# Kernel optimization log

Measured on AMD Instinct MI355X. Metric: run time of the kernel, lower is better.

## Reference

```python
import jax, jax.numpy as jnp
import numpy as np

N, E, D_IN, D_H, D_OUT = 100000, 1600000, 128, 128, 16


def setup_inputs() -> dict:
    key = jax.random.key(0)
    k_x, k_e, k_w1, k_w2 = jax.random.split(key, 4)
    x = jax.random.normal(k_x, (N, D_IN), dtype=jnp.float32)
    edge_index = jax.random.randint(k_e, (2, E), 0, N, dtype=jnp.int64)
    # glorot-ish init for the two GCNConv weight matrices
    W1 = jax.random.normal(k_w1, (D_IN, D_H), dtype=jnp.float32) * (1.0 / np.sqrt(D_IN))
    b1 = jnp.zeros((D_H,), dtype=jnp.float32)
    W2 = jax.random.normal(k_w2, (D_H, D_OUT), dtype=jnp.float32) * (1.0 / np.sqrt(D_H))
    b2 = jnp.zeros((D_OUT,), dtype=jnp.float32)
    return {"x": x, "edge_index": edge_index, "W1": W1, "b1": b1, "W2": W2, "b2": b2}


def _gcn_conv(x, src, dst, norm, W, b, n):
    # linear transform, gather from source nodes, normalize, scatter-add to targets
    h = x @ W                                   # [N, d_out]
    msg = h[src] * norm[:, None]                # [E+N, d_out]
    return jax.ops.segment_sum(msg, dst, num_segments=n) + b


def reference(x, edge_index, W1, b1, W2, b2):
    n = x.shape[0]
    # GCNConv default: add self-loops, symmetric normalization D^-1/2 A D^-1/2
    loops = jnp.arange(n, dtype=edge_index.dtype)
    src = jnp.concatenate([edge_index[0], loops])
    dst = jnp.concatenate([edge_index[1], loops])
    deg = jax.ops.segment_sum(jnp.ones_like(dst, dtype=x.dtype), dst, num_segments=n)
    dinv = jnp.where(deg > 0, jax.lax.rsqrt(deg), 0.0)
    norm = dinv[src] * dinv[dst]                # [E+N]

    h = _gcn_conv(x, src, dst, norm, W1, b1, n)
    h = jax.nn.relu(h)
    # dropout is identity in eval mode (reference uses eval / deterministic path)
    out = _gcn_conv(h, src, dst, norm, W2, b2, n)
    return out
```

## Files before the change

### kernel.cpp

```cpp
#include <hip/hip_runtime.h>

typedef unsigned int uint;
typedef __attribute__((ext_vector_type(8))) short bf16x8;
typedef __attribute__((ext_vector_type(4))) float f32x4;

#define D_IN 128
#define D_H  128
#define D_OUT 16
#define NPC 512
#define NPCSH 9
#define CLDS 224
#define P1 256
#define XL_STRIDE 68
#define WT_STRIDE 68

static __device__ __forceinline__ float bflo(uint u) { return __uint_as_float(u << 16); }
static __device__ __forceinline__ float bfhi(uint u) { return __uint_as_float(u & 0xFFFF0000u); }
static __device__ __forceinline__ uint f2bf(float f) {
    uint b = __float_as_uint(f);
    return (b + 0x7FFFu + ((b >> 16) & 1u)) >> 16;
}
static __device__ __forceinline__ uint pk(float a, float b) {
    return f2bf(a) | (f2bf(b) << 16);
}


__global__ __launch_bounds__(256) void k_p1hist(const int* __restrict__ dst, int E, int N, int C,
                                                int chunk, int* __restrict__ hist1,
                                                const float* __restrict__ W1,
                                                uint* __restrict__ W1p) {
    __shared__ int h[CLDS];
    int t = threadIdx.x, b = blockIdx.x;
    if (b >= P1) {
        int p = (b - P1) * 256 + t;
        int k2 = p >> 7, f = p & 127;
        float w0 = W1[(size_t)(2 * k2) * 128 + f];
        float w1 = W1[(size_t)(2 * k2 + 1) * 128 + f];
        W1p[p] = pk(w0, w1);
        return;
    }
    for (int i = t; i < C; i += 256) h[i] = 0;
    __syncthreads();
    int e0 = b * chunk, e1 = min(e0 + chunk, E);
    for (int e = e0 + t; e < e1; e += 256) {
        int d = dst[e];
        d = max(0, min(d, N - 1));
        atomicAdd(&h[d >> NPCSH], 1);
    }
    __syncthreads();
    for (int i = t; i < C; i += 256) hist1[(size_t)i * P1 + b] = h[i];
}

__global__ __launch_bounds__(1024) void k_p1scan(int* __restrict__ hist1, int C,
                                                 int* __restrict__ cbase) {
    __shared__ int col[CLDS];
    __shared__ int sdata[1024];
    int t = threadIdx.x;
    int w = t >> 6, lane = t & 63;
    for (int i = w; i < C; i += 16) {
        int4 v = ((const int4*)hist1)[i * 64 + lane];
        int s = v.x + v.y + v.z + v.w;
        int inc = s;
        for (int off = 1; off < 64; off <<= 1) {
            int o = __shfl_up(inc, off);
            if (lane >= off) inc += o;
        }
        int excl = inc - s;
        int4 p;
        p.x = excl;
        p.y = excl + v.x;
        p.z = excl + v.x + v.y;
        p.w = excl + v.x + v.y + v.z;
        ((int4*)hist1)[i * 64 + lane] = p;
        if (lane == 63) col[i] = inc;
    }
    __syncthreads();
    int v = (t < C) ? col[t] : 0;
    sdata[t] = v;
    __syncthreads();
    for (int off = 1; off < 1024; off <<= 1) {
        int x = (t >= off) ? sdata[t - off] : 0;
        __syncthreads();
        sdata[t] += x;
        __syncthreads();
    }
    int pos = sdata[t] - v;
    if (t < C) cbase[t] = pos;
    if (t == 1023) cbase[C] = sdata[1023];
    if (t < C) col[t] = pos;
    __syncthreads();
    for (int i = w; i < C; i += 16) {
        int base = col[i];
        int4 p = ((int4*)hist1)[i * 64 + lane];
        p.x += base; p.y += base; p.z += base; p.w += base;
        ((int4*)hist1)[i * 64 + lane] = p;
    }
}

__global__ __launch_bounds__(256) void k_p1fill(const int* __restrict__ src,
                                                const int* __restrict__ dst, int E, int N, int C,
                                                int chunk, const int* __restrict__ hist1,
                                                uint* __restrict__ binned1) {
    __shared__ int cur[CLDS];
    int t = threadIdx.x, b = blockIdx.x;
    for (int i = t; i < C; i += 256) cur[i] = hist1[(size_t)i * P1 + b];
    __syncthreads();
    int e0 = b * chunk, e1 = min(e0 + chunk, E);
    for (int e = e0 + t; e < e1; e += 256) {
        int d = dst[e];
        d = max(0, min(d, N - 1));
        int s = src[e];
        s = max(0, min(s, N - 1));
        int p = atomicAdd(&cur[d >> NPCSH], 1);
        binned1[p] = ((uint)(d & (NPC - 1)) << 17) | (uint)s;
    }
}


__global__ __launch_bounds__(256) void k_p2gemm1(const uint* __restrict__ binned1,
                                                 const int* __restrict__ cbase, int N, int C,
                                                 int* __restrict__ ssrc, int* __restrict__ rowptr,
                                                 int* __restrict__ deg, float* __restrict__ dinv,
                                                 const uint* __restrict__ W1p,
                                                 const float* __restrict__ x,
                                                 uint* __restrict__ hs_b, int ntiles) {
    __shared__ uint smem[128 * WT_STRIDE + 64 * XL_STRIDE];
    int t = threadIdx.x;
    if ((int)blockIdx.x < C) {
        int* ncnt = (int*)smem;
        int* nbase_ = ncnt + NPC;
        int* sdata = nbase_ + NPC;
        int c = blockIdx.x;
        int start = cbase[c], end = cbase[c + 1];
        for (int i = t; i < NPC; i += 256) ncnt[i] = 0;
        __syncthreads();
        for (int j = start + t; j < end; j += 256) atomicAdd(&ncnt[binned1[j] >> 17], 1);
        __syncthreads();
        int v0 = ncnt[2 * t], v1 = ncnt[2 * t + 1];
        int s = v0 + v1;
        sdata[t] = s;
        __syncthreads();
        for (int off = 1; off < 256; off <<= 1) {
            int xv = (t >= off) ? sdata[t - off] : 0;
            __syncthreads();
            sdata[t] += xv;
            __syncthreads();
        }
        int pre = sdata[t] - s;
        nbase_[2 * t] = start + pre;
        nbase_[2 * t + 1] = start + pre + v0;
        __syncthreads();
        for (int i = t; i < NPC; i += 256) {
            int node = c * NPC + i;
            if (node < N) {
                deg[node] = ncnt[i];
                rowptr[node] = nbase_[i];
                dinv[node] = rsqrtf((float)ncnt[i] + 1.0f);
            }
        }
        __syncthreads();
        for (int i = t; i < NPC; i += 256) ncnt[i] = nbase_[i];
        __syncthreads();
        for (int j = start + t; j < end; j += 256) {
            uint pe = binned1[j];
            int p = atomicAdd(&ncnt[pe >> 17], 1);
            ssrc[p] = (int)(pe & 0x1FFFFu);
        }
        return;
    }
    uint* Wt = smem;
    uint* xl = smem + 128 * WT_STRIDE;
    int role = blockIdx.x - C;
    int nroles = gridDim.x - C;
    for (int p = t; p < 64 * 128; p += 256) {
        int k2 = p >> 7, f = p & 127;
        Wt[f * WT_STRIDE + k2] = W1p[p];
    }
    int w = t >> 6, lane = t & 63;
    int q = lane >> 4, m = lane & 15;
    const float4* x4 = (const float4*)x;
    for (int tile = role; tile < ntiles; tile += nroles) {
        int row0 = tile * 64;
        __syncthreads();
        for (int p = t; p < 64 * 32; p += 256) {
            int r = p >> 5, c2 = p & 31;
            int gr = row0 + r;
            float4 v = (gr < N) ? x4[(size_t)gr * 32 + c2] : make_float4(0.f, 0.f, 0.f, 0.f);
            *(uint2*)&xl[r * XL_STRIDE + 2 * c2] = make_uint2(pk(v.x, v.y), pk(v.z, v.w));
        }
        __syncthreads();
        bf16x8 afr[4][4];
#pragma unroll
        for (int rt = 0; rt < 4; rt++)
#pragma unroll
            for (int kc = 0; kc < 4; kc++)
                afr[rt][kc] = *(const bf16x8*)&xl[(rt * 16 + m) * XL_STRIDE + kc * 16 + q * 4];
        f32x4 acc[2][4];
#pragma unroll
        for (int c = 0; c < 2; c++)
#pragma unroll
            for (int rt = 0; rt < 4; rt++) acc[c][rt] = (f32x4){0.f, 0.f, 0.f, 0.f};
#pragma unroll
        for (int c = 0; c < 2; c++) {
            int f = w * 32 + c * 16 + m;
#pragma unroll
            for (int kc = 0; kc < 4; kc++) {
                bf16x8 bfr = *(const bf16x8*)&Wt[f * WT_STRIDE + kc * 16 + q * 4];
#pragma unroll
                for (int rt = 0; rt < 4; rt++)
                    acc[c][rt] = __builtin_amdgcn_mfma_f32_16x16x32_bf16(afr[rt][kc], bfr,
                                                                         acc[c][rt], 0, 0, 0);
            }
        }
        __syncthreads();
        uint* outl = xl;
#pragma unroll
        for (int rt = 0; rt < 4; rt++) {
#pragma unroll
            for (int c = 0; c < 2; c++) {
                f32x4 a = acc[c][rt];
#pragma unroll
                for (int r = 0; r < 4; r++) {
                    float v = a[r];
                    float vn = __shfl_xor(v, 1);
                    if (!(lane & 1)) {
                        int row = rt * 16 + q * 4 + r;
                        int cp = (w * 32 + c * 16 + m) >> 1;
                        outl[row * 65 + cp] = pk(v, vn);
                    }
                }
            }
        }
        __syncthreads();
        for (int p = t; p < 64 * 64; p += 256) {
            int r = p >> 6, cc = p & 63;
            int gr = row0 + r;
            if (gr < N) hs_b[(size_t)gr * 64 + cc] = outl[r * 65 + cc];
        }
    }
}


__global__ __launch_bounds__(256) void k_agg1(const uint* __restrict__ hs_b,
                                              const int* __restrict__ rowptr,
                                              const int* __restrict__ deg,
                                              const int* __restrict__ ssrc,
                                              const float* __restrict__ dinv,
                                              const float2* __restrict__ b1, int N,
                                              uint* __restrict__ rh_b) {
    int w = threadIdx.x >> 6, lane = threadIdx.x & 63;
    int d = blockIdx.x * 4 + w;
    if (d >= N) return;
    int start = rowptr[d], cnt = deg[d];
    float sc = dinv[d];
    uint sv = hs_b[(size_t)d * 64 + lane];
    float a0 = bflo(sv) * sc, a1 = bfhi(sv) * sc;
    int base = 0;
    while (base < cnt) {
        int nb = min(cnt - base, 64);
        int idxv = (lane < nb) ? ssrc[start + base + lane] : 0;
        float dvv = dinv[idxv];
        int j = 0;
        for (; j + 16 <= nb; j += 16) {
            uint u[16];
            float dv[16];
#pragma unroll
            for (int q = 0; q < 16; q++) {
                int i = __shfl(idxv, j + q);
                dv[q] = __shfl(dvv, j + q);
                u[q] = hs_b[(size_t)i * 64 + lane];
            }
#pragma unroll
            for (int q = 0; q < 16; q++) {
                a0 = fmaf(bflo(u[q]), dv[q], a0);
                a1 = fmaf(bfhi(u[q]), dv[q], a1);
            }
        }
        for (; j + 4 <= nb; j += 4) {
            uint u[4];
            float dv[4];
#pragma unroll
            for (int q = 0; q < 4; q++) {
                int i = __shfl(idxv, j + q);
                dv[q] = __shfl(dvv, j + q);
                u[q] = hs_b[(size_t)i * 64 + lane];
            }
#pragma unroll
            for (int q = 0; q < 4; q++) {
                a0 = fmaf(bflo(u[q]), dv[q], a0);
                a1 = fmaf(bfhi(u[q]), dv[q], a1);
            }
        }
        for (; j < nb; j++) {
            int i = __shfl(idxv, j);
            float dv = __shfl(dvv, j);
            uint u = hs_b[(size_t)i * 64 + lane];
            a0 = fmaf(bflo(u), dv, a0);
            a1 = fmaf(bfhi(u), dv, a1);
        }
        base += nb;
    }
    float2 bb = b1[lane];
    rh_b[(size_t)d * 64 + lane] =
        pk(fmaxf(fmaf(a0, sc, bb.x), 0.f), fmaxf(fmaf(a1, sc, bb.y), 0.f));
}


__global__ __launch_bounds__(256) void k_gemm2(const uint* __restrict__ rh_b,
                                               const float* __restrict__ W2,
                                               const float* __restrict__ dinv, int N,
                                               uint* __restrict__ h2_b) {
    __shared__ float Wl[D_H * D_OUT];
    int t = threadIdx.x;
    for (int i = t; i < D_H * D_OUT; i += 256) Wl[i] = W2[i];
    __syncthreads();
    int r = blockIdx.x * 256 + t;
    if (r >= N) return;
    const uint* xrow = rh_b + (size_t)r * 64;
    float acc[16];
#pragma unroll
    for (int f = 0; f < 16; f++) acc[f] = 0.f;
    for (int c = 0; c < 16; c++) {
        uint4 xv = *(const uint4*)(xrow + c * 4);
        uint xs[4] = {xv.x, xv.y, xv.z, xv.w};
#pragma unroll
        for (int u = 0; u < 4; u++) {
            int k = c * 8 + u * 2;
            float x0 = bflo(xs[u]), x1 = bfhi(xs[u]);
            const float* w0 = &Wl[k * 16];
            const float* w1 = &Wl[(k + 1) * 16];
#pragma unroll
            for (int f = 0; f < 16; f++) acc[f] = fmaf(x0, w0[f], acc[f]);
#pragma unroll
            for (int f = 0; f < 16; f++) acc[f] = fmaf(x1, w1[f], acc[f]);
        }
    }
    float sc = dinv[r];
    uint o[8];
#pragma unroll
    for (int q = 0; q < 8; q++) o[q] = pk(acc[2 * q] * sc, acc[2 * q + 1] * sc);
    *(uint4*)&h2_b[(size_t)r * 8] = make_uint4(o[0], o[1], o[2], o[3]);
    *(uint4*)&h2_b[(size_t)r * 8 + 4] = make_uint4(o[4], o[5], o[6], o[7]);
}


__global__ __launch_bounds__(256) void k_agg2(const uint* __restrict__ h2_b,
                                              const int* __restrict__ rowptr,
                                              const int* __restrict__ deg,
                                              const int* __restrict__ ssrc,
                                              const float* __restrict__ dinv,
                                              const float* __restrict__ b2, int N,
                                              float2* __restrict__ out) {
    int w = threadIdx.x >> 6, lane = threadIdx.x & 63;
    int d = blockIdx.x * 4 + w;
    if (d >= N) return;
    int slot = lane >> 3, jp = lane & 7;
    int start = rowptr[d], cnt = deg[d];
    float a0 = 0.f, a1 = 0.f;
    if (slot == 0) {
        uint sv = h2_b[(size_t)d * 8 + jp];
        a0 = bflo(sv);
        a1 = bfhi(sv);
    }
    int base = 0;
    while (base < cnt) {
        int nb = min(cnt - base, 64);
        int idxv = (lane < nb) ? ssrc[start + base + lane] : 0;
        int ng = (nb + 7) >> 3;
        if (ng <= 4) {
            int i0 = __shfl(idxv, slot);
            int i1 = __shfl(idxv, 8 + slot);
            int i2 = __shfl(idxv, 16 + slot);
            int i3 = __shfl(idxv, 24 + slot);
            uint u0 = (slot < nb) ? h2_b[(size_t)i0 * 8 + jp] : 0u;
            uint u1 = (8 + slot < nb) ? h2_b[(size_t)i1 * 8 + jp] : 0u;
            uint u2 = (16 + slot < nb) ? h2_b[(size_t)i2 * 8 + jp] : 0u;
            uint u3 = (24 + slot < nb) ? h2_b[(size_t)i3 * 8 + jp] : 0u;
            a0 += bflo(u0) + bflo(u1) + bflo(u2) + bflo(u3);
            a1 += bfhi(u0) + bfhi(u1) + bfhi(u2) + bfhi(u3);
        } else {
            for (int g = 0; g < ng; g++) {
                int j = g * 8 + slot;
                int i = __shfl(idxv, j);
                if (j < nb) {
                    uint hv = h2_b[(size_t)i * 8 + jp];
                    a0 += bflo(hv);
                    a1 += bfhi(hv);
                }
            }
        }
        base += nb;
    }
    a0 += __shfl_xor(a0, 8);
    a1 += __shfl_xor(a1, 8);
    a0 += __shfl_xor(a0, 16);
    a1 += __shfl_xor(a1, 16);
    a0 += __shfl_xor(a0, 32);
    a1 += __shfl_xor(a1, 32);
    if (slot == 0) {
        float di = dinv[d];
        out[(size_t)d * 8 + jp] =
            make_float2(fmaf(a0, di, b2[2 * jp]), fmaf(a1, di, b2[2 * jp + 1]));
    }
}


extern "C" void kernel_launch(void* const* d_in, const int* in_sizes, int n_in,
                              void* d_out, int out_size, void* d_ws, size_t ws_size,
                              hipStream_t stream) {
    const float* x  = (const float*)d_in[0];
    const int*   ei = (const int*)d_in[1];
    const float* W1 = (const float*)d_in[2];
    const float* b1 = (const float*)d_in[3];
    const float* W2 = (const float*)d_in[4];
    const float* b2 = (const float*)d_in[5];
    int N = in_sizes[0] / D_IN;
    int E = in_sizes[1] / 2;
    const int* src = ei;
    const int* dst = ei + E;
    int C = (N + NPC - 1) / NPC;
    int chunk = (E + P1 - 1) / P1;
    int ntiles = (N + 63) / 64;

    char* ws = (char*)d_ws;
    size_t off = 0;
    auto alloc = [&](size_t bytes) -> char* {
        char* p = ws + off;
        off = (off + bytes + 255) & ~(size_t)255;
        return p;
    };
    int*   hist1   = (int*)alloc((size_t)P1 * C * 4);
    int*   cbase   = (int*)alloc((size_t)(C + 1) * 4);
    uint*  binned1 = (uint*)alloc((size_t)E * 4);
    int*   ssrc    = (int*)alloc((size_t)E * 4);
    int*   rowptr  = (int*)alloc((size_t)N * 4);
    int*   deg     = (int*)alloc((size_t)N * 4);
    float* dinv    = (float*)alloc((size_t)N * 4);
    uint*  W1p     = (uint*)alloc((size_t)64 * 128 * 4);
    uint*  hs_b    = (uint*)alloc((size_t)N * 64 * 4);
    uint*  rh_b    = (uint*)alloc((size_t)N * 64 * 4);
    uint*  h2_b    = hs_b;

    k_p1hist<<<P1 + 32, 256, 0, stream>>>(dst, E, N, C, chunk, hist1, W1, W1p);
    k_p1scan<<<1, 1024, 0, stream>>>(hist1, C, cbase);
    k_p1fill<<<P1, 256, 0, stream>>>(src, dst, E, N, C, chunk, hist1, binned1);
    int g1 = min(768, ntiles);
    k_p2gemm1<<<C + g1, 256, 0, stream>>>(binned1, cbase, N, C, ssrc, rowptr, deg, dinv,
                                          W1p, x, hs_b, ntiles);
    k_agg1<<<(N + 3) / 4, 256, 0, stream>>>(hs_b, rowptr, deg, ssrc, dinv,
                                            (const float2*)b1, N, rh_b);
    k_gemm2<<<(N + 255) / 256, 256, 0, stream>>>(rh_b, W2, dinv, N, h2_b);
    k_agg2<<<(N + 3) / 4, 256, 0, stream>>>(h2_b, rowptr, deg, ssrc, dinv, b2, N,
                                            (float2*)d_out);
}
```

Before: 278.5 us.

## Pre-scale GEMM1 output by dinv and fuse layer-2 GEMM into aggregation

A separate degree kernel now computes deg and dinv before GEMM1, so GEMM1 can scale each output row by dinv[src]. Because rows arrive pre-scaled, the first aggregation drops the per-edge dinv gather and shuffle and becomes a plain sum. That aggregation also applies the 128x16 W2 projection in registers with a wave-wide shuffle reduction, removing the k_gemm2 kernel and the full write and read of the 128-wide relu output. The cost is an extra launch plus a second pass over binned1, and 16 shuffle reductions of six steps each per node.

New measurement: 332.5 us. 1.19x slower.

```diff
diff --git a/kernel.cpp b/kernel.cpp
--- a/kernel.cpp
+++ b/kernel.cpp
@@ -117,10 +117,30 @@
 }
 
 
+__global__ __launch_bounds__(256) void k_deg(const uint* __restrict__ binned1,
+                                             const int* __restrict__ cbase, int N,
+                                             int* __restrict__ deg, float* __restrict__ dinv) {
+    __shared__ int ncnt[NPC];
+    int c = blockIdx.x, t = threadIdx.x;
+    int start = cbase[c], end = cbase[c + 1];
+    for (int i = t; i < NPC; i += 256) ncnt[i] = 0;
+    __syncthreads();
+    for (int j = start + t; j < end; j += 256) atomicAdd(&ncnt[binned1[j] >> 17], 1);
+    __syncthreads();
+    for (int i = t; i < NPC; i += 256) {
+        int node = c * NPC + i;
+        if (node < N) {
+            deg[node] = ncnt[i];
+            dinv[node] = rsqrtf((float)ncnt[i] + 1.0f);
+        }
+    }
+}
+
+
 __global__ __launch_bounds__(256) void k_p2gemm1(const uint* __restrict__ binned1,
                                                  const int* __restrict__ cbase, int N, int C,
                                                  int* __restrict__ ssrc, int* __restrict__ rowptr,
-                                                 int* __restrict__ deg, float* __restrict__ dinv,
+                                                 const float* __restrict__ dinv,
                                                  const uint* __restrict__ W1p,
                                                  const float* __restrict__ x,
                                                  uint* __restrict__ hs_b, int ntiles) {
@@ -152,11 +172,7 @@
         __syncthreads();
         for (int i = t; i < NPC; i += 256) {
             int node = c * NPC + i;
-            if (node < N) {
-                deg[node] = ncnt[i];
-                rowptr[node] = nbase_[i];
-                dinv[node] = rsqrtf((float)ncnt[i] + 1.0f);
-            }
+            if (node < N) rowptr[node] = nbase_[i];
         }
         __syncthreads();
         for (int i = t; i < NPC; i += 256) ncnt[i] = nbase_[i];
@@ -216,12 +232,23 @@
         uint* outl = xl;
 #pragma unroll
         for (int rt = 0; rt < 4; rt++) {
+            int gb = row0 + rt * 16 + q * 4;
+            float4 dv;
+            if (gb + 3 < N) {
+                dv = *(const float4*)&dinv[gb];
+            } else {
+                dv.x = (gb < N) ? dinv[gb] : 0.f;
+                dv.y = (gb + 1 < N) ? dinv[gb + 1] : 0.f;
+                dv.z = (gb + 2 < N) ? dinv[gb + 2] : 0.f;
+                dv.w = (gb + 3 < N) ? dinv[gb + 3] : 0.f;
+            }
+            float dr[4] = {dv.x, dv.y, dv.z, dv.w};
 #pragma unroll
             for (int c = 0; c < 2; c++) {
                 f32x4 a = acc[c][rt];
 #pragma unroll
                 for (int r = 0; r < 4; r++) {
-                    float v = a[r];
+                    float v = a[r] * dr[r];
                     float vn = __shfl_xor(v, 1);
                     if (!(lane & 1)) {
                         int row = rt * 16 + q * 4 + r;
@@ -241,106 +268,80 @@
 }
 
 
-__global__ __launch_bounds__(256) void k_agg1(const uint* __restrict__ hs_b,
-                                              const int* __restrict__ rowptr,
-                                              const int* __restrict__ deg,
-                                              const int* __restrict__ ssrc,
-                                              const float* __restrict__ dinv,
-                                              const float2* __restrict__ b1, int N,
-                                              uint* __restrict__ rh_b) {
+__global__ __launch_bounds__(256) void k_agg1g2(const uint* __restrict__ hs_b,
+                                                const int* __restrict__ rowptr,
+                                                const int* __restrict__ deg,
+                                                const int* __restrict__ ssrc,
+                                                const float* __restrict__ dinv,
+                                                const float2* __restrict__ b1,
+                                                const float* __restrict__ W2, int N,
+                                                uint* __restrict__ h2_b) {
     int w = threadIdx.x >> 6, lane = threadIdx.x & 63;
     int d = blockIdx.x * 4 + w;
     if (d >= N) return;
     int start = rowptr[d], cnt = deg[d];
-    float sc = dinv[d];
     uint sv = hs_b[(size_t)d * 64 + lane];
-    float a0 = bflo(sv) * sc, a1 = bfhi(sv) * sc;
+    float a0 = bflo(sv), a1 = bfhi(sv);
     int base = 0;
     while (base < cnt) {
         int nb = min(cnt - base, 64);
         int idxv = (lane < nb) ? ssrc[start + base + lane] : 0;
-        float dvv = dinv[idxv];
         int j = 0;
         for (; j + 16 <= nb; j += 16) {
             uint u[16];
-            float dv[16];
 #pragma unroll
             for (int q = 0; q < 16; q++) {
                 int i = __shfl(idxv, j + q);
-                dv[q] = __shfl(dvv, j + q);
                 u[q] = hs_b[(size_t)i * 64 + lane];
             }
 #pragma unroll
             for (int q = 0; q < 16; q++) {
-                a0 = fmaf(bflo(u[q]), dv[q], a0);
-                a1 = fmaf(bfhi(u[q]), dv[q], a1);
+                a0 += bflo(u[q]);
+                a1 += bfhi(u[q]);
             }
         }
         for (; j + 4 <= nb; j += 4) {
             uint u[4];
-            float dv[4];
 #pragma unroll
             for (int q = 0; q < 4; q++) {
                 int i = __shfl(idxv, j + q);
-                dv[q] = __shfl(dvv, j + q);
                 u[q] = hs_b[(size_t)i * 64 + lane];
             }
 #pragma unroll
             for (int q = 0; q < 4; q++) {
-                a0 = fmaf(bflo(u[q]), dv[q], a0);
-                a1 = fmaf(bfhi(u[q]), dv[q], a1);
+                a0 += bflo(u[q]);
+                a1 += bfhi(u[q]);
             }
         }
         for (; j < nb; j++) {
             int i = __shfl(idxv, j);
-            float dv = __shfl(dvv, j);
             uint u = hs_b[(size_t)i * 64 + lane];
-            a0 = fmaf(bflo(u), dv, a0);
-            a1 = fmaf(bfhi(u), dv, a1);
+            a0 += bflo(u);
+            a1 += bfhi(u);
         }
         base += nb;
     }
+    float sc = dinv[d];
     float2 bb = b1[lane];
-    rh_b[(size_t)d * 64 + lane] =
-        pk(fmaxf(fmaf(a0, sc, bb.x), 0.f), fmaxf(fmaf(a1, sc, bb.y), 0.f));
-}
-
-
-__global__ __launch_bounds__(256) void k_gemm2(const uint* __restrict__ rh_b,
-                                               const float* __restrict__ W2,
-                                               const float* __restrict__ dinv, int N,
-                                               uint* __restrict__ h2_b) {
-    __shared__ float Wl[D_H * D_OUT];
-    int t = threadIdx.x;
-    for (int i = t; i < D_H * D_OUT; i += 256) Wl[i] = W2[i];
-    __syncthreads();
-    int r = blockIdx.x * 256 + t;
-    if (r >= N) return;
-    const uint* xrow = rh_b + (size_t)r * 64;
-    float acc[16];
-#pragma unroll
-    for (int f = 0; f < 16; f++) acc[f] = 0.f;
-    for (int c = 0; c < 16; c++) {
-        uint4 xv = *(const uint4*)(xrow + c * 4);
-        uint xs[4] = {xv.x, xv.y, xv.z, xv.w};
-#pragma unroll
-        for (int u = 0; u < 4; u++) {
-            int k = c * 8 + u * 2;
-            float x0 = bflo(xs[u]), x1 = bfhi(xs[u]);
-            const float* w0 = &Wl[k * 16];
-            const float* w1 = &Wl[(k + 1) * 16];
-#pragma unroll
-            for (int f = 0; f < 16; f++) acc[f] = fmaf(x0, w0[f], acc[f]);
-#pragma unroll
-            for (int f = 0; f < 16; f++) acc[f] = fmaf(x1, w1[f], acc[f]);
-        }
-    }
-    float sc = dinv[r];
-    uint o[8];
-#pragma unroll
-    for (int q = 0; q < 8; q++) o[q] = pk(acc[2 * q] * sc, acc[2 * q + 1] * sc);
-    *(uint4*)&h2_b[(size_t)r * 8] = make_uint4(o[0], o[1], o[2], o[3]);
-    *(uint4*)&h2_b[(size_t)r * 8 + 4] = make_uint4(o[4], o[5], o[6], o[7]);
+    float r0 = fmaxf(fmaf(a0, sc, bb.x), 0.f);
+    float r1 = fmaxf(fmaf(a1, sc, bb.y), 0.f);
+    const float4* w2v = (const float4*)(W2 + (size_t)lane * 32);
+    float p[16];
+#pragma unroll
+    for (int g4 = 0; g4 < 4; g4++) {
+        float4 wa = w2v[g4];
+        float4 wb = w2v[4 + g4];
+        p[4 * g4 + 0] = fmaf(r0, wa.x, r1 * wb.x);
+        p[4 * g4 + 1] = fmaf(r0, wa.y, r1 * wb.y);
+        p[4 * g4 + 2] = fmaf(r0, wa.z, r1 * wb.z);
+        p[4 * g4 + 3] = fmaf(r0, wa.w, r1 * wb.w);
+    }
+#pragma unroll
+    for (int off = 1; off < 64; off <<= 1) {
+#pragma unroll
+        for (int f = 0; f < 16; f++) p[f] += __shfl_xor(p[f], off);
+    }
+    if (lane < 8) h2_b[(size_t)d * 8 + lane] = pk(p[2 * lane] * sc, p[2 * lane + 1] * sc);
 }
 
 
@@ -439,17 +440,17 @@
     uint*  W1p     = (uint*)alloc((size_t)64 * 128 * 4);
     uint*  hs_b    = (uint*)alloc((size_t)N * 64 * 4);
     uint*  rh_b    = (uint*)alloc((size_t)N * 64 * 4);
-    uint*  h2_b    = hs_b;
+    uint*  h2_b    = rh_b;
 
     k_p1hist<<<P1 + 32, 256, 0, stream>>>(dst, E, N, C, chunk, hist1, W1, W1p);
     k_p1scan<<<1, 1024, 0, stream>>>(hist1, C, cbase);
     k_p1fill<<<P1, 256, 0, stream>>>(src, dst, E, N, C, chunk, hist1, binned1);
+    k_deg<<<C, 256, 0, stream>>>(binned1, cbase, N, deg, dinv);
     int g1 = min(768, ntiles);
-    k_p2gemm1<<<C + g1, 256, 0, stream>>>(binned1, cbase, N, C, ssrc, rowptr, deg, dinv,
+    k_p2gemm1<<<C + g1, 256, 0, stream>>>(binned1, cbase, N, C, ssrc, rowptr, dinv,
                                           W1p, x, hs_b, ntiles);
-    k_agg1<<<(N + 3) / 4, 256, 0, stream>>>(hs_b, rowptr, deg, ssrc, dinv,
-                                            (const float2*)b1, N, rh_b);
-    k_gemm2<<<(N + 255) / 256, 256, 0, stream>>>(rh_b, W2, dinv, N, h2_b);
+    k_agg1g2<<<(N + 3) / 4, 256, 0, stream>>>(hs_b, rowptr, deg, ssrc, dinv,
+                                              (const float2*)b1, W2, N, h2_b);
     k_agg2<<<(N + 3) / 4, 256, 0, stream>>>(h2_b, rowptr, deg, ssrc, dinv, b2, N,
                                             (float2*)d_out);
 }
```

## Prescale GEMM1 output rows by dinv to drop per-edge scaling in aggregation

Applied to the files above, without the earlier changes.

Adds a small degree kernel that computes deg and dinv before GEMM1, so the GEMM1 epilogue can multiply each output row by its source dinv before storing bf16. The layer-1 aggregation then becomes a plain sum of gathered rows, with no per-edge dinv gather and no shuffle of dinv values, and the destination dinv is applied once at the end. In exchange it adds a kernel launch that rereads binned1, and prescaling before bf16 rounding slightly changes numerics.

Measured after the change: 292.7 us. 5.1% more time.

```diff
diff --git a/kernel.cpp b/kernel.cpp
--- a/kernel.cpp
+++ b/kernel.cpp
@@ -117,10 +117,30 @@
 }
 
 
+__global__ __launch_bounds__(256) void k_deg(const uint* __restrict__ binned1,
+                                             const int* __restrict__ cbase, int N,
+                                             int* __restrict__ deg, float* __restrict__ dinv) {
+    __shared__ int ncnt[NPC];
+    int c = blockIdx.x, t = threadIdx.x;
+    int start = cbase[c], end = cbase[c + 1];
+    for (int i = t; i < NPC; i += 256) ncnt[i] = 0;
+    __syncthreads();
+    for (int j = start + t; j < end; j += 256) atomicAdd(&ncnt[binned1[j] >> 17], 1);
+    __syncthreads();
+    for (int i = t; i < NPC; i += 256) {
+        int node = c * NPC + i;
+        if (node < N) {
+            deg[node] = ncnt[i];
+            dinv[node] = rsqrtf((float)ncnt[i] + 1.0f);
+        }
+    }
+}
+
+
 __global__ __launch_bounds__(256) void k_p2gemm1(const uint* __restrict__ binned1,
                                                  const int* __restrict__ cbase, int N, int C,
                                                  int* __restrict__ ssrc, int* __restrict__ rowptr,
-                                                 int* __restrict__ deg, float* __restrict__ dinv,
+                                                 const float* __restrict__ dinv,
                                                  const uint* __restrict__ W1p,
                                                  const float* __restrict__ x,
                                                  uint* __restrict__ hs_b, int ntiles) {
@@ -152,11 +172,7 @@
         __syncthreads();
         for (int i = t; i < NPC; i += 256) {
             int node = c * NPC + i;
-            if (node < N) {
-                deg[node] = ncnt[i];
-                rowptr[node] = nbase_[i];
-                dinv[node] = rsqrtf((float)ncnt[i] + 1.0f);
-            }
+            if (node < N) rowptr[node] = nbase_[i];
         }
         __syncthreads();
         for (int i = t; i < NPC; i += 256) ncnt[i] = nbase_[i];
@@ -216,12 +232,23 @@
         uint* outl = xl;
 #pragma unroll
         for (int rt = 0; rt < 4; rt++) {
+            int gb = row0 + rt * 16 + q * 4;
+            float4 dv;
+            if (gb + 3 < N) {
+                dv = *(const float4*)&dinv[gb];
+            } else {
+                dv.x = (gb < N) ? dinv[gb] : 0.f;
+                dv.y = (gb + 1 < N) ? dinv[gb + 1] : 0.f;
+                dv.z = (gb + 2 < N) ? dinv[gb + 2] : 0.f;
+                dv.w = (gb + 3 < N) ? dinv[gb + 3] : 0.f;
+            }
+            float dr[4] = {dv.x, dv.y, dv.z, dv.w};
 #pragma unroll
             for (int c = 0; c < 2; c++) {
                 f32x4 a = acc[c][rt];
 #pragma unroll
                 for (int r = 0; r < 4; r++) {
-                    float v = a[r];
+                    float v = a[r] * dr[r];
                     float vn = __shfl_xor(v, 1);
                     if (!(lane & 1)) {
                         int row = rt * 16 + q * 4 + r;
@@ -252,54 +279,48 @@
     int d = blockIdx.x * 4 + w;
     if (d >= N) return;
     int start = rowptr[d], cnt = deg[d];
-    float sc = dinv[d];
     uint sv = hs_b[(size_t)d * 64 + lane];
-    float a0 = bflo(sv) * sc, a1 = bfhi(sv) * sc;
+    float a0 = bflo(sv), a1 = bfhi(sv);
     int base = 0;
     while (base < cnt) {
         int nb = min(cnt - base, 64);
         int idxv = (lane < nb) ? ssrc[start + base + lane] : 0;
-        float dvv = dinv[idxv];
         int j = 0;
         for (; j + 16 <= nb; j += 16) {
             uint u[16];
-            float dv[16];
 #pragma unroll
             for (int q = 0; q < 16; q++) {
                 int i = __shfl(idxv, j + q);
-                dv[q] = __shfl(dvv, j + q);
                 u[q] = hs_b[(size_t)i * 64 + lane];
             }
 #pragma unroll
             for (int q = 0; q < 16; q++) {
-                a0 = fmaf(bflo(u[q]), dv[q], a0);
-                a1 = fmaf(bfhi(u[q]), dv[q], a1);
+                a0 += bflo(u[q]);
+                a1 += bfhi(u[q]);
             }
         }
         for (; j + 4 <= nb; j += 4) {
             uint u[4];
-            float dv[4];
 #pragma unroll
             for (int q = 0; q < 4; q++) {
                 int i = __shfl(idxv, j + q);
-                dv[q] = __shfl(dvv, j + q);
                 u[q] = hs_b[(size_t)i * 64 + lane];
             }
 #pragma unroll
             for (int q = 0; q < 4; q++) {
-                a0 = fmaf(bflo(u[q]), dv[q], a0);
-                a1 = fmaf(bfhi(u[q]), dv[q], a1);
+                a0 += bflo(u[q]);
+                a1 += bfhi(u[q]);
             }
         }
         for (; j < nb; j++) {
             int i = __shfl(idxv, j);
-            float dv = __shfl(dvv, j);
             uint u = hs_b[(size_t)i * 64 + lane];
-            a0 = fmaf(bflo(u), dv, a0);
-            a1 = fmaf(bfhi(u), dv, a1);
+            a0 += bflo(u);
+            a1 += bfhi(u);
         }
         base += nb;
     }
+    float sc = dinv[d];
     float2 bb = b1[lane];
     rh_b[(size_t)d * 64 + lane] =
         pk(fmaxf(fmaf(a0, sc, bb.x), 0.f), fmaxf(fmaf(a1, sc, bb.y), 0.f));
@@ -444,8 +465,9 @@
     k_p1hist<<<P1 + 32, 256, 0, stream>>>(dst, E, N, C, chunk, hist1, W1, W1p);
     k_p1scan<<<1, 1024, 0, stream>>>(hist1, C, cbase);
     k_p1fill<<<P1, 256, 0, stream>>>(src, dst, E, N, C, chunk, hist1, binned1);
+    k_deg<<<C, 256, 0, stream>>>(binned1, cbase, N, deg, dinv);
     int g1 = min(768, ntiles);
-    k_p2gemm1<<<C + g1, 256, 0, stream>>>(binned1, cbase, N, C, ssrc, rowptr, deg, dinv,
+    k_p2gemm1<<<C + g1, 256, 0, stream>>>(binned1, cbase, N, C, ssrc, rowptr, dinv,
                                           W1p, x, hs_b, ntiles);
     k_agg1<<<(N + 3) / 4, 256, 0, stream>>>(hs_b, rowptr, deg, ssrc, dinv,
                                             (const float2*)b1, N, rh_b);
```

## Fuse second-layer GEMM into layer-1 aggregation kernel

Applied to the files above, without the earlier changes.

Merges the layer-2 linear transform into the layer-1 aggregation kernel. Each wave keeps its ReLU'd hidden row in LDS and computes the 16 outputs via a dot product against a pre-transposed W2, which is built in an extra block of the histogram kernel. This removes writing and re-reading the full bf16 hidden activation buffer and one kernel launch. It adds per-wave LDS traffic and shuffle reductions to the aggregation kernel, and keeps the hidden row in fp32 rather than bf16 before the GEMM.

Result: slower. 318.2 us (+14.3%).

```diff
diff --git a/kernel.cpp b/kernel.cpp
--- a/kernel.cpp
+++ b/kernel.cpp
@@ -28,9 +28,18 @@
 __global__ __launch_bounds__(256) void k_p1hist(const int* __restrict__ dst, int E, int N, int C,
                                                 int chunk, int* __restrict__ hist1,
                                                 const float* __restrict__ W1,
-                                                uint* __restrict__ W1p) {
+                                                uint* __restrict__ W1p,
+                                                const float* __restrict__ W2,
+                                                float* __restrict__ W2t) {
     __shared__ int h[CLDS];
     int t = threadIdx.x, b = blockIdx.x;
+    if (b >= P1 + 32) {
+        for (int p = t; p < D_H * D_OUT; p += 256) {
+            int f = p >> 7, k = p & 127;
+            W2t[p] = W2[k * 16 + f];
+        }
+        return;
+    }
     if (b >= P1) {
         int p = (b - P1) * 256 + t;
         int k2 = p >> 7, f = p & 127;
@@ -241,13 +250,15 @@
 }
 
 
-__global__ __launch_bounds__(256) void k_agg1(const uint* __restrict__ hs_b,
-                                              const int* __restrict__ rowptr,
-                                              const int* __restrict__ deg,
-                                              const int* __restrict__ ssrc,
-                                              const float* __restrict__ dinv,
-                                              const float2* __restrict__ b1, int N,
-                                              uint* __restrict__ rh_b) {
+__global__ __launch_bounds__(256) void k_agg1g2(const uint* __restrict__ hs_b,
+                                                const int* __restrict__ rowptr,
+                                                const int* __restrict__ deg,
+                                                const int* __restrict__ ssrc,
+                                                const float* __restrict__ dinv,
+                                                const float2* __restrict__ b1,
+                                                const float* __restrict__ W2t, int N,
+                                                uint* __restrict__ h2_b) {
+    __shared__ float rhs[4][128];
     int w = threadIdx.x >> 6, lane = threadIdx.x & 63;
     int d = blockIdx.x * 4 + w;
     if (d >= N) return;
@@ -301,46 +312,27 @@
         base += nb;
     }
     float2 bb = b1[lane];
-    rh_b[(size_t)d * 64 + lane] =
-        pk(fmaxf(fmaf(a0, sc, bb.x), 0.f), fmaxf(fmaf(a1, sc, bb.y), 0.f));
-}
-
-
-__global__ __launch_bounds__(256) void k_gemm2(const uint* __restrict__ rh_b,
-                                               const float* __restrict__ W2,
-                                               const float* __restrict__ dinv, int N,
-                                               uint* __restrict__ h2_b) {
-    __shared__ float Wl[D_H * D_OUT];
-    int t = threadIdx.x;
-    for (int i = t; i < D_H * D_OUT; i += 256) Wl[i] = W2[i];
-    __syncthreads();
-    int r = blockIdx.x * 256 + t;
-    if (r >= N) return;
-    const uint* xrow = rh_b + (size_t)r * 64;
-    float acc[16];
-#pragma unroll
-    for (int f = 0; f < 16; f++) acc[f] = 0.f;
-    for (int c = 0; c < 16; c++) {
-        uint4 xv = *(const uint4*)(xrow + c * 4);
-        uint xs[4] = {xv.x, xv.y, xv.z, xv.w};
-#pragma unroll
-        for (int u = 0; u < 4; u++) {
-            int k = c * 8 + u * 2;
-            float x0 = bflo(xs[u]), x1 = bfhi(xs[u]);
-            const float* w0 = &Wl[k * 16];
-            const float* w1 = &Wl[(k + 1) * 16];
-#pragma unroll
-            for (int f = 0; f < 16; f++) acc[f] = fmaf(x0, w0[f], acc[f]);
-#pragma unroll
-            for (int f = 0; f < 16; f++) acc[f] = fmaf(x1, w1[f], acc[f]);
-        }
-    }
-    float sc = dinv[r];
-    uint o[8];
-#pragma unroll
-    for (int q = 0; q < 8; q++) o[q] = pk(acc[2 * q] * sc, acc[2 * q + 1] * sc);
-    *(uint4*)&h2_b[(size_t)r * 8] = make_uint4(o[0], o[1], o[2], o[3]);
-    *(uint4*)&h2_b[(size_t)r * 8 + 4] = make_uint4(o[4], o[5], o[6], o[7]);
+    float r0 = fmaxf(fmaf(a0, sc, bb.x), 0.f);
+    float r1 = fmaxf(fmaf(a1, sc, bb.y), 0.f);
+    ((float2*)rhs[w])[lane] = make_float2(r0, r1);
+    int f = lane & 15, kc = lane >> 4;
+    const float4* rp = (const float4*)&rhs[w][kc * 32];
+    const float4* wt = (const float4*)(W2t + (size_t)f * 128 + kc * 32);
+    float pacc = 0.f;
+#pragma unroll
+    for (int j8 = 0; j8 < 8; j8++) {
+        float4 rv = rp[j8];
+        float4 wv = wt[j8];
+        pacc = fmaf(rv.x, wv.x, pacc);
+        pacc = fmaf(rv.y, wv.y, pacc);
+        pacc = fmaf(rv.z, wv.z, pacc);
+        pacc = fmaf(rv.w, wv.w, pacc);
+    }
+    pacc += __shfl_xor(pacc, 16);
+    pacc += __shfl_xor(pacc, 32);
+    float pn = __shfl_xor(pacc, 1);
+    if (lane < 16 && !(lane & 1))
+        h2_b[(size_t)d * 8 + (lane >> 1)] = pk(pacc * sc, pn * sc);
 }
 
 
@@ -437,19 +429,18 @@
     int*   deg     = (int*)alloc((size_t)N * 4);
     float* dinv    = (float*)alloc((size_t)N * 4);
     uint*  W1p     = (uint*)alloc((size_t)64 * 128 * 4);
+    float* W2t     = (float*)alloc((size_t)D_H * D_OUT * 4);
     uint*  hs_b    = (uint*)alloc((size_t)N * 64 * 4);
-    uint*  rh_b    = (uint*)alloc((size_t)N * 64 * 4);
-    uint*  h2_b    = hs_b;
-
-    k_p1hist<<<P1 + 32, 256, 0, stream>>>(dst, E, N, C, chunk, hist1, W1, W1p);
+    uint*  h2_b    = (uint*)alloc((size_t)N * 8 * 4);
+
+    k_p1hist<<<P1 + 33, 256, 0, stream>>>(dst, E, N, C, chunk, hist1, W1, W1p, W2, W2t);
     k_p1scan<<<1, 1024, 0, stream>>>(hist1, C, cbase);
     k_p1fill<<<P1, 256, 0, stream>>>(src, dst, E, N, C, chunk, hist1, binned1);
     int g1 = min(768, ntiles);
     k_p2gemm1<<<C + g1, 256, 0, stream>>>(binned1, cbase, N, C, ssrc, rowptr, deg, dinv,
                                           W1p, x, hs_b, ntiles);
-    k_agg1<<<(N + 3) / 4, 256, 0, stream>>>(hs_b, rowptr, deg, ssrc, dinv,
-                                            (const float2*)b1, N, rh_b);
-    k_gemm2<<<(N + 255) / 256, 256, 0, stream>>>(rh_b, W2, dinv, N, h2_b);
+    k_agg1g2<<<(N + 3) / 4, 256, 0, stream>>>(hs_b, rowptr, deg, ssrc, dinv,
+                                              (const float2*)b1, W2t, N, h2_b);
     k_agg2<<<(N + 3) / 4, 256, 0, stream>>>(h2_b, rowptr, deg, ssrc, dinv, b2, N,
                                             (float2*)d_out);
 }
```
